# Optimization experiments

Hardware: AMD Instinct MI355X
Metric: run time of the kernel (lower is better)

Reference implementation:

```python
import jax, jax.numpy as jnp
import numpy as np

H_DIM = 1024
NUM_HEADS = 16
HEAD_DIM = H_DIM // NUM_HEADS
EPS = 1e-5


def rms_norm(x, w, eps=EPS):
    var = jnp.mean(jnp.square(x), axis=-1, keepdims=True)
    return x * jax.lax.rsqrt(var + eps) * w


def setup_inputs() -> dict:
    key = jax.random.key(0)
    ks = jax.random.split(key, 8)
    B, S = 2, 2048
    x = jax.random.normal(ks[0], (B, S, H_DIM), dtype=jnp.float32)
    # learned params (orthogonal init approximated by scaled normal for a correctness baseline)
    qkv_w = jax.random.normal(ks[1], (3 * H_DIM, H_DIM), dtype=jnp.float32) / np.sqrt(H_DIM)
    gate_w = jax.random.normal(ks[2], (NUM_HEADS, H_DIM), dtype=jnp.float32) / np.sqrt(H_DIM)
    o_w = jax.random.normal(ks[3], (H_DIM, H_DIM), dtype=jnp.float32) / np.sqrt(H_DIM)
    prenorm_w = jnp.ones((H_DIM,), dtype=jnp.float32)
    q_norm_w = jnp.ones((HEAD_DIM,), dtype=jnp.float32)
    k_norm_w = jnp.ones((HEAD_DIM,), dtype=jnp.float32)
    return {"x": x, "prenorm_w": prenorm_w, "qkv_w": qkv_w, "gate_w": gate_w,
            "o_w": o_w, "q_norm_w": q_norm_w, "k_norm_w": k_norm_w}


def reference(x, prenorm_w, qkv_w, gate_w, o_w, q_norm_w, k_norm_w):
    B, S, D = x.shape
    residual = x
    xn = rms_norm(x, prenorm_w)                                   # [B,S,D]
    qkv = jnp.einsum('bsd,ed->bse', xn, qkv_w)                    # [B,S,3D]
    qkv = qkv.reshape(B, S, 3, NUM_HEADS, HEAD_DIM)
    gate = jnp.einsum('bsd,hd->bsh', xn, gate_w)                  # [B,S,H]
    q, k, v = qkv[:, :, 0], qkv[:, :, 1], qkv[:, :, 2]            # [B,S,H,hd]
    q = rms_norm(q, q_norm_w)
    k = rms_norm(k, k_norm_w)
    scale = 1.0 / np.sqrt(HEAD_DIM).astype(np.float32)
    scores = jnp.einsum('bqhd,bkhd->bhqk', q, k) * scale          # [B,H,S,S]
    attn = jax.nn.softmax(scores, axis=-1)
    out = jnp.einsum('bhqk,bkhd->bhqd', attn, v)                  # [B,H,S,hd]
    out = out * jax.nn.sigmoid(gate).transpose(0, 2, 1)[..., None]
    out = out.transpose(0, 2, 1, 3).reshape(B, S, D)              # [B,S,D]
    return jnp.einsum('bsd,ed->bse', out, o_w) + residual
```

## Files before the change

### kernel.cpp

```cpp
#include <hip/hip_runtime.h>
#include <math.h>

typedef __bf16 bf16x8 __attribute__((ext_vector_type(8)));
typedef float f32x4 __attribute__((ext_vector_type(4)));
typedef unsigned short ushort_t;

#define SEQ 2048
#define MROWS 4096
#define EPS 1e-5f
#define QKS 3200
#define LOG2E 1.4426950408889634f
#define SMAX_B2 17.32f

#if __has_builtin(__builtin_amdgcn_exp2f)
#define EXP2(x) __builtin_amdgcn_exp2f(x)
#else
#define EXP2(x) exp2f(x)
#endif

__device__ __forceinline__ float bf2f(ushort_t u) {
  union { unsigned int i; float f; } c; c.i = ((unsigned int)u) << 16; return c.f;
}
__device__ __forceinline__ ushort_t f2bf(float f) {
  union { unsigned int i; float f; } c; c.f = f;
  unsigned int i = c.i;
  unsigned int r = i + 0x7fffu + ((i >> 16) & 1u);
  return (ushort_t)(r >> 16);
}
__device__ __forceinline__ ushort_t f2bf_fast(float f) {
  union { __bf16 b; ushort_t u; } cv; cv.b = (__bf16)f; return cv.u;
}

__device__ __forceinline__ float wave_sum(float v) {
  #pragma unroll
  for (int off = 32; off > 0; off >>= 1) v += __shfl_xor(v, off);
  return v;
}

__global__ void detect_kernel(const unsigned int* __restrict__ xraw, int* __restrict__ flag) {
  int tid = threadIdx.x;
  int cnt = 0;
  for (int i = tid; i < 4096; i += 256) {
    unsigned int e = (xraw[i] >> 7) & 0xFFu;
    cnt += (e >= 100u && e <= 150u) ? 1 : 0;
  }
  __shared__ int sred[256];
  sred[tid] = cnt;
  __syncthreads();
  for (int s = 128; s > 0; s >>= 1) {
    if (tid < s) sred[tid] += sred[tid + s];
    __syncthreads();
  }
  if (tid == 0) flag[0] = (sred[0] > 2048) ? 1 : 0;
}

__global__ void prep_kernel(const void* __restrict__ qkvw_in, const void* __restrict__ gw_in,
                            const void* __restrict__ ow_in, const void* __restrict__ pw_in,
                            const void* __restrict__ qn_in, const void* __restrict__ kn_in,
                            ushort_t* __restrict__ Wcat, ushort_t* __restrict__ ow,
                            float* __restrict__ pwf, float* __restrict__ qnf,
                            float* __restrict__ knf, const int* __restrict__ flag) {
  int bid = blockIdx.x, tid = threadIdx.x;
  int bf = *flag;
  if (bid < 12288) {
    int i = bid * 256 + tid;
    Wcat[i] = bf ? ((const ushort_t*)qkvw_in)[i] : f2bf(((const float*)qkvw_in)[i]);
  } else if (bid < 12352) {
    int i = (bid - 12288) * 256 + tid;
    Wcat[3072 * 1024 + i] = bf ? ((const ushort_t*)gw_in)[i] : f2bf(((const float*)gw_in)[i]);
  } else if (bid < 16448) {
    int i = (bid - 12352) * 256 + tid;
    ow[i] = bf ? ((const ushort_t*)ow_in)[i] : f2bf(((const float*)ow_in)[i]);
  } else {
    for (int i = tid; i < 1024; i += 256)
      pwf[i] = bf ? bf2f(((const ushort_t*)pw_in)[i]) : ((const float*)pw_in)[i];
    if (tid < 64) {
      qnf[tid] = bf ? bf2f(((const ushort_t*)qn_in)[tid]) : ((const float*)qn_in)[tid];
      knf[tid] = bf ? bf2f(((const ushort_t*)kn_in)[tid]) : ((const float*)kn_in)[tid];
    }
  }
}

__global__ void prenorm_kernel(const void* __restrict__ xraw,
                               const float* __restrict__ w,
                               ushort_t* __restrict__ xn,
                               const int* __restrict__ flag) {
  int row = blockIdx.x;
  int tid = threadIdx.x;
  float4 u;
  if (*flag) {
    ushort4 s = ((const ushort4*)xraw)[row * 256 + tid];
    u.x = bf2f(s.x); u.y = bf2f(s.y); u.z = bf2f(s.z); u.w = bf2f(s.w);
  } else {
    u = ((const float4*)xraw)[row * 256 + tid];
  }
  float ss = u.x*u.x + u.y*u.y + u.z*u.z + u.w*u.w;
  ss = wave_sum(ss);
  __shared__ float red[4];
  if ((tid & 63) == 0) red[tid >> 6] = ss;
  __syncthreads();
  float total = red[0] + red[1] + red[2] + red[3];
  float inv = rsqrtf(total * (1.0f / 1024.0f) + EPS);
  float4 wu = ((const float4*)w)[tid];
  ushort4 o;
  o.x = f2bf(u.x * inv * wu.x);
  o.y = f2bf(u.y * inv * wu.y);
  o.z = f2bf(u.z * inv * wu.z);
  o.w = f2bf(u.w * inv * wu.w);
  ((ushort4*)(xn + (long long)row * 1024))[tid] = o;
}

__device__ __forceinline__ void gll16(const ushort_t* g, ushort_t* l) {
  __builtin_amdgcn_global_load_lds(
      (const __attribute__((address_space(1))) unsigned int*)g,
      (__attribute__((address_space(3))) unsigned int*)l, 16, 0, 0);
}

__global__ void gemm_qkv_fused(const ushort_t* __restrict__ A, const ushort_t* __restrict__ B,
                               ushort_t* __restrict__ C, float* __restrict__ gate,
                               const float* __restrict__ qw, const float* __restrict__ kw) {
  __shared__ ushort_t As[128 * 32];
  __shared__ ushort_t Bs[128 * 32];
  int tid = threadIdx.x, wave = tid >> 6, lane = tid & 63;
  int m_blk = blockIdx.y * 128, n_blk = blockIdx.x * 128;
  int wm = (wave & 1) * 64, wn = (wave >> 1) * 64;
  int g = lane >> 4, c = lane & 15;
  int arow = lane >> 2;
  int akc = (lane & 3) << 3;
  f32x4 acc[4][4] = {};
  for (int kt = 0; kt < 1024; kt += 32) {
    #pragma unroll
    for (int i = 0; i < 2; ++i) {
      int rbase = (i * 4 + wave) * 16;
      gll16(A + (long long)(m_blk + rbase + arow) * 1024 + kt + akc, &As[rbase * 32]);
      gll16(B + (long long)(n_blk + rbase + arow) * 1024 + kt + akc, &Bs[rbase * 32]);
    }
    __syncthreads();
    bf16x8 af[4], bfr[4];
    #pragma unroll
    for (int mi = 0; mi < 4; ++mi)
      af[mi] = *(const bf16x8*)&As[(wm + mi * 16 + c) * 32 + (g << 3)];
    #pragma unroll
    for (int ni = 0; ni < 4; ++ni)
      bfr[ni] = *(const bf16x8*)&Bs[(wn + ni * 16 + c) * 32 + (g << 3)];
    #pragma unroll
    for (int mi = 0; mi < 4; ++mi)
      #pragma unroll
      for (int ni = 0; ni < 4; ++ni)
        acc[mi][ni] = __builtin_amdgcn_mfma_f32_16x16x32_bf16(af[mi], bfr[ni], acc[mi][ni], 0, 0, 0);
    __syncthreads();
  }
  int col_base = n_blk + wn;
  if (col_base < 2048) {
    int isk = col_base >= 1024;
    float scale = isk ? 1.0f : (0.125f * LOG2E);
    const float* nw = isk ? kw : qw;
    float w[4];
    #pragma unroll
    for (int ni = 0; ni < 4; ++ni) w[ni] = nw[ni * 16 + c];
    #pragma unroll
    for (int mi = 0; mi < 4; ++mi)
      #pragma unroll
      for (int r = 0; r < 4; ++r) {
        float ss = 0.f;
        #pragma unroll
        for (int ni = 0; ni < 4; ++ni) ss += acc[mi][ni][r] * acc[mi][ni][r];
        #pragma unroll
        for (int off = 8; off > 0; off >>= 1) ss += __shfl_xor(ss, off);
        float inv = rsqrtf(ss * (1.0f / 64.0f) + EPS) * scale;
        int row = m_blk + wm + mi * 16 + g * 4 + r;
        #pragma unroll
        for (int ni = 0; ni < 4; ++ni)
          C[(long long)row * QKS + col_base + ni * 16 + c] = f2bf(acc[mi][ni][r] * inv * w[ni]);
      }
  } else if (col_base < 3072) {
    #pragma unroll
    for (int mi = 0; mi < 4; ++mi)
      #pragma unroll
      for (int r = 0; r < 4; ++r) {
        int row = m_blk + wm + mi * 16 + g * 4 + r;
        #pragma unroll
        for (int ni = 0; ni < 4; ++ni)
          C[(long long)row * QKS + col_base + ni * 16 + c] = f2bf(acc[mi][ni][r]);
      }
  } else if (col_base == 3072) {
    #pragma unroll
    for (int mi = 0; mi < 4; ++mi)
      #pragma unroll
      for (int r = 0; r < 4; ++r) {
        int row = m_blk + wm + mi * 16 + g * 4 + r;
        float v = acc[mi][0][r];
        gate[(long long)row * 16 + c] = 1.0f / (1.0f + __expf(-v));
      }
  }
}

__global__ void gemm_tiled(const ushort_t* __restrict__ A, const ushort_t* __restrict__ B,
                           void* __restrict__ Cv, const void* __restrict__ res,
                           const int* __restrict__ flag,
                           int K, int lda, int ldb, int ldc) {
  __shared__ ushort_t As[128 * 32];
  __shared__ ushort_t Bs[128 * 32];
  int tid = threadIdx.x, wave = tid >> 6, lane = tid & 63;
  int m_blk = blockIdx.y * 128, n_blk = blockIdx.x * 128;
  int wm = (wave & 1) * 64, wn = (wave >> 1) * 64;
  int g = lane >> 4, c = lane & 15;
  int arow = lane >> 2;
  int akc = (lane & 3) << 3;
  f32x4 acc[4][4] = {};
  for (int kt = 0; kt < K; kt += 32) {
    #pragma unroll
    for (int i = 0; i < 2; ++i) {
      int rbase = (i * 4 + wave) * 16;
      gll16(A + (long long)(m_blk + rbase + arow) * lda + kt + akc, &As[rbase * 32]);
      gll16(B + (long long)(n_blk + rbase + arow) * ldb + kt + akc, &Bs[rbase * 32]);
    }
    __syncthreads();
    bf16x8 af[4], bfr[4];
    #pragma unroll
    for (int mi = 0; mi < 4; ++mi)
      af[mi] = *(const bf16x8*)&As[(wm + mi * 16 + c) * 32 + (g << 3)];
    #pragma unroll
    for (int ni = 0; ni < 4; ++ni)
      bfr[ni] = *(const bf16x8*)&Bs[(wn + ni * 16 + c) * 32 + (g << 3)];
    #pragma unroll
    for (int mi = 0; mi < 4; ++mi)
      #pragma unroll
      for (int ni = 0; ni < 4; ++ni)
        acc[mi][ni] = __builtin_amdgcn_mfma_f32_16x16x32_bf16(af[mi], bfr[ni], acc[mi][ni], 0, 0, 0);
    __syncthreads();
  }
  int outbf = flag ? *flag : 1;
  #pragma unroll
  for (int mi = 0; mi < 4; ++mi)
    #pragma unroll
    for (int ni = 0; ni < 4; ++ni)
      #pragma unroll
      for (int r = 0; r < 4; ++r) {
        int row = m_blk + wm + mi * 16 + g * 4 + r;
        int col = n_blk + wn + ni * 16 + c;
        long long idx = (long long)row * ldc + col;
        float v = acc[mi][ni][r];
        if (res) v += outbf ? bf2f(((const ushort_t*)res)[idx]) : ((const float*)res)[idx];
        if (outbf) ((ushort_t*)Cv)[idx] = f2bf(v);
        else       ((float*)Cv)[idx] = v;
      }
}

__global__ void vt_kernel(const ushort_t* __restrict__ qkv, ushort_t* __restrict__ Vt) {
  __shared__ ushort_t tile[64][65];
  int s0 = blockIdx.x * 64;
  int bh = blockIdx.y;
  int b = bh >> 4, h = bh & 15;
  const ushort_t* src = qkv + (long long)b * SEQ * QKS + 2048 + h * 64;
  int d = threadIdx.x & 63, srow = threadIdx.x >> 6;
  #pragma unroll
  for (int i = 0; i < 16; ++i) {
    int sl = i * 4 + srow;
    tile[sl][d] = src[(long long)(s0 + sl) * QKS + d];
  }
  __syncthreads();
  ushort_t* dst = Vt + (long long)bh * 64 * SEQ + s0;
  int sl2 = threadIdx.x & 63, drow = threadIdx.x >> 6;
  #pragma unroll
  for (int i = 0; i < 16; ++i) {
    int dd = i * 4 + drow;
    dst[(long long)dd * SEQ + sl2] = tile[sl2][dd];
  }
}

__global__ void flash_kernel(const ushort_t* __restrict__ qkv, const ushort_t* __restrict__ Vt,
                             const float* __restrict__ gate, ushort_t* __restrict__ ao) {
  __shared__ ushort_t Ks[64 * 64];
  __shared__ ushort_t Vs[64 * 64];
  __shared__ ushort_t Ps[4][16 * 64];
  int tid = threadIdx.x, wave = tid >> 6, lane = tid & 63;
  int g = lane >> 4, c = lane & 15;
  int q0 = blockIdx.x * 64;
  int bh = blockIdx.y, b = bh >> 4, h = bh & 15;
  const ushort_t* qbase = qkv + (long long)b * SEQ * QKS + h * 64;
  const ushort_t* kbase = qbase + 1024;
  const ushort_t* vtbase = Vt + (long long)bh * 64 * SEQ;
  int qrow = q0 + wave * 16 + c;
  bf16x8 qa0 = *(const bf16x8*)(qbase + (long long)qrow * QKS + (g << 3));
  bf16x8 qa1 = *(const bf16x8*)(qbase + (long long)qrow * QKS + 32 + (g << 3));
  f32x4 accO[4] = {};
  float l_p[4] = {0.f, 0.f, 0.f, 0.f};
  int srow = lane >> 3;
  int schk = lane & 7;
  for (int s0 = 0; s0 < SEQ; s0 += 64) {
    #pragma unroll
    for (int t = 0; t < 2; ++t) {
      int rb = t * 32 + wave * 8;
      int row = rb + srow;
      int gch = (schk ^ (row & 7)) << 3;
      gll16(kbase + (long long)(s0 + row) * QKS + gch, &Ks[rb * 64]);
      gll16(vtbase + (long long)row * SEQ + s0 + gch, &Vs[rb * 64]);
    }
    __syncthreads();
    f32x4 sacc[4] = {};
    #pragma unroll
    for (int ni = 0; ni < 4; ++ni) {
      int n = ni * 16 + c;
      bf16x8 kb0 = *(const bf16x8*)&Ks[n * 64 + ((g ^ (n & 7)) << 3)];
      bf16x8 kb1 = *(const bf16x8*)&Ks[n * 64 + (((4 + g) ^ (n & 7)) << 3)];
      sacc[ni] = __builtin_amdgcn_mfma_f32_16x16x32_bf16(qa0, kb0, sacc[ni], 0, 0, 0);
      sacc[ni] = __builtin_amdgcn_mfma_f32_16x16x32_bf16(qa1, kb1, sacc[ni], 0, 0, 0);
    }
    #pragma unroll
    for (int r = 0; r < 4; ++r) {
      int q = g * 4 + r;
      int sw = (q & 7) << 3;
      #pragma unroll
      for (int ni = 0; ni < 4; ++ni) {
        float p = EXP2(sacc[ni][r] - SMAX_B2);
        l_p[r] += p;
        int col = ni * 16 + c;
        Ps[wave][q * 64 + ((col & 56) ^ sw) + (col & 7)] = f2bf_fast(p);
      }
    }
    bf16x8 pa0 = *(const bf16x8*)&Ps[wave][c * 64 + ((g ^ (c & 7)) << 3)];
    bf16x8 pa1 = *(const bf16x8*)&Ps[wave][c * 64 + (((4 + g) ^ (c & 7)) << 3)];
    #pragma unroll
    for (int di = 0; di < 4; ++di) {
      int n = di * 16 + c;
      bf16x8 vb0 = *(const bf16x8*)&Vs[n * 64 + ((g ^ (n & 7)) << 3)];
      bf16x8 vb1 = *(const bf16x8*)&Vs[n * 64 + (((4 + g) ^ (n & 7)) << 3)];
      accO[di] = __builtin_amdgcn_mfma_f32_16x16x32_bf16(pa0, vb0, accO[di], 0, 0, 0);
      accO[di] = __builtin_amdgcn_mfma_f32_16x16x32_bf16(pa1, vb1, accO[di], 0, 0, 0);
    }
    __syncthreads();
  }
  #pragma unroll
  for (int r = 0; r < 4; ++r) {
    #pragma unroll
    for (int off = 8; off > 0; off >>= 1) l_p[r] += __shfl_xor(l_p[r], off);
    int row = q0 + wave * 16 + g * 4 + r;
    float sg = gate[(long long)(b * SEQ + row) * 16 + h];
    float scale = sg / l_p[r];
    #pragma unroll
    for (int di = 0; di < 4; ++di) {
      int col = h * 64 + di * 16 + c;
      ao[(long long)(b * SEQ + row) * 1024 + col] = f2bf_fast(accO[di][r] * scale);
    }
  }
}

extern "C" void kernel_launch(void* const* d_in, const int* in_sizes, int n_in,
                              void* d_out, int out_size, void* d_ws, size_t ws_size,
                              hipStream_t stream) {
  (void)in_sizes; (void)n_in; (void)out_size; (void)ws_size;
  char* ws = (char*)d_ws;
  ushort_t* Wcat = (ushort_t*)(ws);
  ushort_t* ow   = (ushort_t*)(ws + (7ll << 20));
  float*    pwf  = (float*)   (ws + (9ll << 20));
  float*    qnf  = (float*)   (ws + (9ll << 20) + (8 << 10));
  float*    knf  = (float*)   (ws + (9ll << 20) + (12 << 10));
  int*      flag = (int*)     (ws + (9ll << 20) + (16 << 10));
  float*    gate = (float*)   (ws + (9ll << 20) + (64 << 10));
  ushort_t* xn   = (ushort_t*)(ws + (10ll << 20));
  ushort_t* qkv2 = (ushort_t*)(ws + (18ll << 20));
  ushort_t* Vt   = (ushort_t*)(ws + (44ll << 20));
  ushort_t* ao   = (ushort_t*)(ws + (52ll << 20));

  detect_kernel<<<1, 256, 0, stream>>>((const unsigned int*)d_in[0], flag);
  prep_kernel<<<16449, 256, 0, stream>>>(d_in[2], d_in[3], d_in[4], d_in[1], d_in[5], d_in[6],
                                         Wcat, ow, pwf, qnf, knf, flag);
  prenorm_kernel<<<MROWS, 256, 0, stream>>>(d_in[0], pwf, xn, flag);
  gemm_qkv_fused<<<dim3(25, 32), 256, 0, stream>>>(xn, Wcat, qkv2, gate, qnf, knf);
  vt_kernel<<<dim3(32, 32), 256, 0, stream>>>(qkv2, Vt);
  flash_kernel<<<dim3(32, 32), 256, 0, stream>>>(qkv2, Vt, gate, ao);
  gemm_tiled<<<dim3(8, 32), 256, 0, stream>>>(ao, ow, d_out, d_in[0], flag,
                                              1024, 1024, 1024, 1024);
}
```

Measured before the change: 240.5 us.

## Double-buffer K/V tiles in flash kernel and raise MFMA wave priority

Doubles the K and V LDS buffers so the async global-to-LDS load of the next 64-key tile is issued before computing on the current tile. This overlaps memory latency with the QK and PV MFMA work and halves the number of full-block waits on loads. It also wraps the MFMA loops in s_setprio hints. The cost is double the K/V shared memory, which may reduce occupancy, and correctness now depends on the async loads completing before the barrier.

```diff
diff --git a/kernel.cpp b/kernel.cpp
--- a/kernel.cpp
+++ b/kernel.cpp
@@ -271,8 +271,8 @@
 
 __global__ void flash_kernel(const ushort_t* __restrict__ qkv, const ushort_t* __restrict__ Vt,
                              const float* __restrict__ gate, ushort_t* __restrict__ ao) {
-  __shared__ ushort_t Ks[64 * 64];
-  __shared__ ushort_t Vs[64 * 64];
+  __shared__ ushort_t Ks[2][64 * 64];
+  __shared__ ushort_t Vs[2][64 * 64];
   __shared__ ushort_t Ps[4][16 * 64];
   int tid = threadIdx.x, wave = tid >> 6, lane = tid & 63;
   int g = lane >> 4, c = lane & 15;
@@ -288,49 +288,68 @@
   float l_p[4] = {0.f, 0.f, 0.f, 0.f};
   int srow = lane >> 3;
   int schk = lane & 7;
-  for (int s0 = 0; s0 < SEQ; s0 += 64) {
-    #pragma unroll
-    for (int t = 0; t < 2; ++t) {
-      int rb = t * 32 + wave * 8;
-      int row = rb + srow;
-      int gch = (schk ^ (row & 7)) << 3;
-      gll16(kbase + (long long)(s0 + row) * QKS + gch, &Ks[rb * 64]);
-      gll16(vtbase + (long long)row * SEQ + s0 + gch, &Vs[rb * 64]);
-    }
-    __syncthreads();
-    f32x4 sacc[4] = {};
-    #pragma unroll
-    for (int ni = 0; ni < 4; ++ni) {
-      int n = ni * 16 + c;
-      bf16x8 kb0 = *(const bf16x8*)&Ks[n * 64 + ((g ^ (n & 7)) << 3)];
-      bf16x8 kb1 = *(const bf16x8*)&Ks[n * 64 + (((4 + g) ^ (n & 7)) << 3)];
-      sacc[ni] = __builtin_amdgcn_mfma_f32_16x16x32_bf16(qa0, kb0, sacc[ni], 0, 0, 0);
-      sacc[ni] = __builtin_amdgcn_mfma_f32_16x16x32_bf16(qa1, kb1, sacc[ni], 0, 0, 0);
-    }
-    #pragma unroll
-    for (int r = 0; r < 4; ++r) {
-      int q = g * 4 + r;
-      int sw = (q & 7) << 3;
-      #pragma unroll
-      for (int ni = 0; ni < 4; ++ni) {
-        float p = EXP2(sacc[ni][r] - SMAX_B2);
-        l_p[r] += p;
-        int col = ni * 16 + c;
-        Ps[wave][q * 64 + ((col & 56) ^ sw) + (col & 7)] = f2bf_fast(p);
-      }
-    }
-    bf16x8 pa0 = *(const bf16x8*)&Ps[wave][c * 64 + ((g ^ (c & 7)) << 3)];
-    bf16x8 pa1 = *(const bf16x8*)&Ps[wave][c * 64 + (((4 + g) ^ (c & 7)) << 3)];
-    #pragma unroll
-    for (int di = 0; di < 4; ++di) {
-      int n = di * 16 + c;
-      bf16x8 vb0 = *(const bf16x8*)&Vs[n * 64 + ((g ^ (n & 7)) << 3)];
-      bf16x8 vb1 = *(const bf16x8*)&Vs[n * 64 + (((4 + g) ^ (n & 7)) << 3)];
-      accO[di] = __builtin_amdgcn_mfma_f32_16x16x32_bf16(pa0, vb0, accO[di], 0, 0, 0);
-      accO[di] = __builtin_amdgcn_mfma_f32_16x16x32_bf16(pa1, vb1, accO[di], 0, 0, 0);
-    }
-    __syncthreads();
-  }
+
+  #define STAGE(BUF, S0) do {                                                        \
+    _Pragma("unroll")                                                                \
+    for (int t = 0; t < 2; ++t) {                                                    \
+      int rb = t * 32 + wave * 8;                                                    \
+      int row = rb + srow;                                                           \
+      int gch = (schk ^ (row & 7)) << 3;                                             \
+      gll16(kbase + (long long)((S0) + row) * QKS + gch, &Ks[BUF][rb * 64]);         \
+      gll16(vtbase + (long long)row * SEQ + (S0) + gch, &Vs[BUF][rb * 64]);          \
+    } } while (0)
+
+  #define COMPUTE(BUF) do {                                                          \
+    f32x4 sacc[4] = {};                                                              \
+    __builtin_amdgcn_s_setprio(1);                                                   \
+    _Pragma("unroll")                                                                \
+    for (int ni = 0; ni < 4; ++ni) {                                                 \
+      int n = ni * 16 + c;                                                           \
+      bf16x8 kb0 = *(const bf16x8*)&Ks[BUF][n * 64 + ((g ^ (n & 7)) << 3)];          \
+      bf16x8 kb1 = *(const bf16x8*)&Ks[BUF][n * 64 + (((4 + g) ^ (n & 7)) << 3)];    \
+      sacc[ni] = __builtin_amdgcn_mfma_f32_16x16x32_bf16(qa0, kb0, sacc[ni], 0, 0, 0); \
+      sacc[ni] = __builtin_amdgcn_mfma_f32_16x16x32_bf16(qa1, kb1, sacc[ni], 0, 0, 0); \
+    }                                                                                \
+    __builtin_amdgcn_s_setprio(0);                                                   \
+    _Pragma("unroll")                                                                \
+    for (int r = 0; r < 4; ++r) {                                                    \
+      int q = g * 4 + r;                                                             \
+      int sw = (q & 7) << 3;                                                         \
+      _Pragma("unroll")                                                              \
+      for (int ni = 0; ni < 4; ++ni) {                                               \
+        float p = EXP2(sacc[ni][r] - SMAX_B2);                                       \
+        l_p[r] += p;                                                                 \
+        int col = ni * 16 + c;                                                       \
+        Ps[wave][q * 64 + ((col & 56) ^ sw) + (col & 7)] = f2bf_fast(p);             \
+      }                                                                              \
+    }                                                                                \
+    bf16x8 pa0 = *(const bf16x8*)&Ps[wave][c * 64 + ((g ^ (c & 7)) << 3)];           \
+    bf16x8 pa1 = *(const bf16x8*)&Ps[wave][c * 64 + (((4 + g) ^ (c & 7)) << 3)];     \
+    __builtin_amdgcn_s_setprio(1);                                                   \
+    _Pragma("unroll")                                                                \
+    for (int di = 0; di < 4; ++di) {                                                 \
+      int n = di * 16 + c;                                                           \
+      bf16x8 vb0 = *(const bf16x8*)&Vs[BUF][n * 64 + ((g ^ (n & 7)) << 3)];          \
+      bf16x8 vb1 = *(const bf16x8*)&Vs[BUF][n * 64 + (((4 + g) ^ (n & 7)) << 3)];    \
+      accO[di] = __builtin_amdgcn_mfma_f32_16x16x32_bf16(pa0, vb0, accO[di], 0, 0, 0); \
+      accO[di] = __builtin_amdgcn_mfma_f32_16x16x32_bf16(pa1, vb1, accO[di], 0, 0, 0); \
+    }                                                                                \
+    __builtin_amdgcn_s_setprio(0);                                                   \
+  } while (0)
+
+  STAGE(0, 0);
+  __syncthreads();
+  for (int s0 = 0; s0 < SEQ; s0 += 128) {
+    STAGE(1, s0 + 64);
+    COMPUTE(0);
+    __syncthreads();
+    if (s0 + 128 < SEQ) STAGE(0, s0 + 128);
+    COMPUTE(1);
+    __syncthreads();
+  }
+  #undef STAGE
+  #undef COMPUTE
+
   #pragma unroll
   for (int r = 0; r < 4; ++r) {
     #pragma unroll
```

Result: no change. 240.9 us (+0.1%).
